# Kernel optimization log

Hardware: AMD Instinct MI355X
Metric: run time of the kernel (lower is better)

The kernel has to match this reference:

```python
import jax, jax.numpy as jnp
import numpy as np

IN_FEATS = 768   # xlm-roberta-base hidden size
HIDDEN = 128     # hardcoded in GCNEncoder
OUT_FEATS = 128
NUM_GRAPHS = 1024
NODES_PER_GRAPH = 256
N = NUM_GRAPHS * NODES_PER_GRAPH
N_CLASS = 2


def setup_inputs() -> dict:
    key = jax.random.key(0)
    ks = jax.random.split(key, 12)
    s = lambda fan_in: 1.0 / np.sqrt(fan_in)
    return {
        "x": jax.random.normal(ks[0], (N, IN_FEATS), dtype=jnp.float32),
        "prompt_node": jax.random.normal(ks[1], (IN_FEATS,), dtype=jnp.float32),
        "class_nodes": jax.random.normal(ks[2], (N_CLASS, IN_FEATS), dtype=jnp.float32),
        "W1": jax.random.uniform(ks[3], (IN_FEATS, HIDDEN), jnp.float32, -s(IN_FEATS), s(IN_FEATS)),
        "b1": jnp.zeros((HIDDEN,), jnp.float32),
        "W2": jax.random.uniform(ks[4], (HIDDEN, OUT_FEATS), jnp.float32, -s(HIDDEN), s(HIDDEN)),
        "b2": jnp.zeros((OUT_FEATS,), jnp.float32),
        "Wfc": jax.random.uniform(ks[5], (OUT_FEATS, N_CLASS), jnp.float32, -s(OUT_FEATS), s(OUT_FEATS)),
        "bfc": jnp.zeros((N_CLASS,), jnp.float32),
        "num_graphs": NUM_GRAPHS,
    }


def _gcn_conv(h_in, W, b, src, dst, num_nodes):
    # PyG GCNConv: add self loops, symmetric norm D^-1/2 (A+I) D^-1/2, then X W + b.
    deg = jax.ops.segment_sum(jnp.ones_like(src, dtype=h_in.dtype), dst,
                              num_segments=num_nodes) + 1.0  # +1 for self loop
    dinv = deg ** -0.5
    h = h_in @ W                                    # [num_nodes, out]
    norm = dinv[src] * dinv[dst]                    # [E]
    agg = jax.ops.segment_sum(h[src] * norm[:, None], dst, num_segments=num_nodes)
    agg = agg + (dinv * dinv)[:, None] * h          # self-loop contribution
    return agg + b


def reference(x, prompt_node, class_nodes, W1, b1, W2, b2, Wfc, bfc, num_graphs):
    G = int(num_graphs)
    N_orig = x.shape[0]
    n_per = N_orig // G
    n_cls = class_nodes.shape[0]
    total = N_orig + G + G * n_cls

    # construct_prompted_graph: append prompt nodes then class nodes (tiled per graph)
    full_x = jnp.concatenate([
        x,
        jnp.broadcast_to(prompt_node, (G, prompt_node.shape[0])),
        jnp.tile(class_nodes, (G, 1)),
    ], axis=0)

    # star edges: node -> prompt, prompt -> class; then to_undirected (both dirs)
    src1 = jnp.arange(N_orig)
    dst1 = N_orig + jnp.repeat(jnp.arange(G), n_per)
    src2 = jnp.repeat(N_orig + jnp.arange(G), n_cls)
    dst2 = N_orig + G + jnp.arange(G * n_cls)
    src = jnp.concatenate([src1, src2, dst1, dst2])
    dst = jnp.concatenate([dst1, dst2, src1, src2])

    h = _gcn_conv(full_x, W1, b1, src, dst, total)
    h = jax.nn.relu(h)  # dropout omitted (eval mode)
    h = _gcn_conv(h, W2, b2, src, dst, total)

    class_idx = N_orig + G + jnp.arange(G * n_cls)
    class_emb = h[class_idx]                         # [G*n_cls, OUT_FEATS]
    logits = class_emb @ Wfc + bfc                   # [G*n_cls, 2]
    return jax.nn.log_softmax(logits, axis=-1)
```

## Files before the change

### kernel.cpp

```cpp
#include <hip/hip_runtime.h>
#include <math.h>

namespace {
constexpr int IN_FEATS = 768;
constexpr int HIDDEN   = 128;
constexpr int G        = 1024;
constexpr int NPG      = 256;
constexpr int C4       = IN_FEATS / 4;
constexpr int NT       = 384;
constexpr int GPB      = 2;
constexpr int NB       = G / GPB;
typedef float f32x4 __attribute__((ext_vector_type(4)));
}

__global__ __launch_bounds__(NT, 3) void fused_kernel(
    const float* __restrict__ x, const float* __restrict__ prompt,
    const float* __restrict__ cls,
    const float* __restrict__ W1, const float* __restrict__ b1,
    const float* __restrict__ W2, const float* __restrict__ b2,
    const float* __restrict__ Wfc, const float* __restrict__ bfc,
    float* __restrict__ out)
{
    __shared__ __align__(16) float S[GPB][IN_FEATS];
    __shared__ f32x4  partA[2][C4];
    __shared__ float  pb[3][5][HIDDEN];
    __shared__ __align__(16) float rbuf[4][HIDDEN];
    __shared__ float  red[2][2];

    const int g0  = blockIdx.x * GPB;
    const int tid = threadIdx.x;
    const float ainv = 1.0f / sqrtf(518.0f);

    const int p  = tid / C4;
    const int c4 = tid % C4;
    const f32x4* xb = reinterpret_cast<const f32x4*>(x);
    for (int gg = 0; gg < GPB; ++gg) {
        const f32x4* xp = xb + ((size_t)(g0 + gg) * NPG + p) * C4 + c4;
        f32x4 a0 = (f32x4)0.0f;
        f32x4 a1 = a0, a2 = a0, a3 = a0;
        for (int i = 0; i < NPG / 2; i += 4) {
            const f32x4 v0 = __builtin_nontemporal_load(xp + (size_t)(2 * (i + 0)) * C4);
            const f32x4 v1 = __builtin_nontemporal_load(xp + (size_t)(2 * (i + 1)) * C4);
            const f32x4 v2 = __builtin_nontemporal_load(xp + (size_t)(2 * (i + 2)) * C4);
            const f32x4 v3 = __builtin_nontemporal_load(xp + (size_t)(2 * (i + 3)) * C4);
            a0 += v0; a1 += v1; a2 += v2; a3 += v3;
        }
        partA[p][c4] = (a0 + a1) + (a2 + a3);
        __syncthreads();
        if (tid < C4) {
            const f32x4 q0 = partA[0][tid], q1 = partA[1][tid];
            *reinterpret_cast<f32x4*>(&S[gg][tid * 4]) = q0 + q1;
        }
        __syncthreads();
    }

    {
        const int seg = tid >> 7;
        const int j   = tid & (HIDDEN - 1);
        const int cb  = seg * 256;
        const float* w1p = W1 + (size_t)cb * HIDDEN + j;
        float t0 = 0.f, t1 = 0.f, hp = 0.f, h0 = 0.f, h1 = 0.f;
        for (int cc = 0; cc < 256; cc += 4) {
            const int c = cb + cc;
            const f32x4 s0 = *reinterpret_cast<const f32x4*>(&S[0][c]);
            const f32x4 s1 = *reinterpret_cast<const f32x4*>(&S[1][c]);
            const f32x4 pv = *reinterpret_cast<const f32x4*>(prompt + c);
            const f32x4 k0 = *reinterpret_cast<const f32x4*>(cls + c);
            const f32x4 k1 = *reinterpret_cast<const f32x4*>(cls + IN_FEATS + c);
            const float w0 = w1p[(size_t)(cc + 0) * HIDDEN];
            const float w1 = w1p[(size_t)(cc + 1) * HIDDEN];
            const float w2 = w1p[(size_t)(cc + 2) * HIDDEN];
            const float w3 = w1p[(size_t)(cc + 3) * HIDDEN];
            t0 = fmaf(s0.x, w0, t0); t1 = fmaf(s1.x, w0, t1);
            hp = fmaf(pv.x, w0, hp); h0 = fmaf(k0.x, w0, h0); h1 = fmaf(k1.x, w0, h1);
            t0 = fmaf(s0.y, w1, t0); t1 = fmaf(s1.y, w1, t1);
            hp = fmaf(pv.y, w1, hp); h0 = fmaf(k0.y, w1, h0); h1 = fmaf(k1.y, w1, h1);
            t0 = fmaf(s0.z, w2, t0); t1 = fmaf(s1.z, w2, t1);
            hp = fmaf(pv.z, w2, hp); h0 = fmaf(k0.z, w2, h0); h1 = fmaf(k1.z, w2, h1);
            t0 = fmaf(s0.w, w3, t0); t1 = fmaf(s1.w, w3, t1);
            hp = fmaf(pv.w, w3, hp); h0 = fmaf(k0.w, w3, h0); h1 = fmaf(k1.w, w3, h1);
        }
        pb[seg][0][j] = t0; pb[seg][1][j] = t1;
        pb[seg][2][j] = hp; pb[seg][3][j] = h0; pb[seg][4][j] = h1;
    }
    __syncthreads();
    if (tid < HIDDEN) {
        const float t0 = pb[0][0][tid] + pb[1][0][tid] + pb[2][0][tid];
        const float t1 = pb[0][1][tid] + pb[1][1][tid] + pb[2][1][tid];
        const float hp = pb[0][2][tid] + pb[1][2][tid] + pb[2][2][tid];
        const float h0 = pb[0][3][tid] + pb[1][3][tid] + pb[2][3][tid];
        const float h1 = pb[0][4][tid] + pb[1][4][tid] + pb[2][4][tid];
        const float b  = b1[tid];
        const float C1 = ainv * (h0 + h1) + hp * (1.0f / 259.0f) + b;
        rbuf[0][tid] = fmaxf(fmaf(ainv, t0, C1), 0.f);
        rbuf[1][tid] = fmaxf(fmaf(ainv, t1, C1), 0.f);
        rbuf[2][tid] = fmaxf(fmaf(ainv, hp, fmaf(0.5f, h0, b)), 0.f);
        rbuf[3][tid] = fmaxf(fmaf(ainv, hp, fmaf(0.5f, h1, b)), 0.f);
    }
    __syncthreads();

    float u0 = 0.f, u1 = 0.f, uc0 = 0.f, uc1 = 0.f;
    if (tid < HIDDEN) {
        const float* w2p = W2 + tid;
        for (int c = 0; c < HIDDEN; c += 4) {
            const f32x4 r0 = *reinterpret_cast<const f32x4*>(&rbuf[0][c]);
            const f32x4 r1 = *reinterpret_cast<const f32x4*>(&rbuf[1][c]);
            const f32x4 q0 = *reinterpret_cast<const f32x4*>(&rbuf[2][c]);
            const f32x4 q1 = *reinterpret_cast<const f32x4*>(&rbuf[3][c]);
            const float wa = w2p[(size_t)(c + 0) * HIDDEN];
            const float wb = w2p[(size_t)(c + 1) * HIDDEN];
            const float wc = w2p[(size_t)(c + 2) * HIDDEN];
            const float wd = w2p[(size_t)(c + 3) * HIDDEN];
            u0  = fmaf(r0.x, wa, u0);  u1  = fmaf(r1.x, wa, u1);
            uc0 = fmaf(q0.x, wa, uc0); uc1 = fmaf(q1.x, wa, uc1);
            u0  = fmaf(r0.y, wb, u0);  u1  = fmaf(r1.y, wb, u1);
            uc0 = fmaf(q0.y, wb, uc0); uc1 = fmaf(q1.y, wb, uc1);
            u0  = fmaf(r0.z, wc, u0);  u1  = fmaf(r1.z, wc, u1);
            uc0 = fmaf(q0.z, wc, uc0); uc1 = fmaf(q1.z, wc, uc1);
            u0  = fmaf(r0.w, wd, u0);  u1  = fmaf(r1.w, wd, u1);
            uc0 = fmaf(q0.w, wd, uc0); uc1 = fmaf(q1.w, wd, uc1);
        }
    }

    const float bfc0 = bfc[0], bfc1 = bfc[1];
    for (int gg = 0; gg < GPB; ++gg) {
        for (int k = 0; k < 2; ++k) {
            float p0 = 0.f, p1 = 0.f;
            if (tid < HIDDEN) {
                const float ug = (gg == 0) ? u0 : u1;
                const float uk = (k == 0) ? uc0 : uc1;
                const float v  = fmaf(ainv, ug, fmaf(0.5f, uk, b2[tid]));
                p0 = v * Wfc[tid * 2 + 0];
                p1 = v * Wfc[tid * 2 + 1];
                #pragma unroll
                for (int off = 32; off > 0; off >>= 1) {
                    p0 += __shfl_down(p0, off);
                    p1 += __shfl_down(p1, off);
                }
                if ((tid & 63) == 0) { red[tid >> 6][0] = p0; red[tid >> 6][1] = p1; }
            }
            __syncthreads();
            if (tid == 0) {
                const float l0 = red[0][0] + red[1][0] + bfc0;
                const float l1 = red[0][1] + red[1][1] + bfc1;
                const float m   = fmaxf(l0, l1);
                const float lse = m + logf(expf(l0 - m) + expf(l1 - m));
                float* o = out + ((size_t)(g0 + gg) * 2 + k) * 2;
                o[0] = l0 - lse;
                o[1] = l1 - lse;
            }
            __syncthreads();
        }
    }
}

extern "C" void kernel_launch(void* const* d_in, const int* in_sizes, int n_in,
                              void* d_out, int out_size, void* d_ws, size_t ws_size,
                              hipStream_t stream) {
    const float* x      = (const float*)d_in[0];
    const float* prompt = (const float*)d_in[1];
    const float* cls    = (const float*)d_in[2];
    const float* W1     = (const float*)d_in[3];
    const float* b1     = (const float*)d_in[4];
    const float* W2     = (const float*)d_in[5];
    const float* b2     = (const float*)d_in[6];
    const float* Wfc    = (const float*)d_in[7];
    const float* bfc    = (const float*)d_in[8];
    float* out = (float*)d_out;

    fused_kernel<<<NB, NT, 0, stream>>>(x, prompt, cls, W1, b1, W2, b2,
                                        Wfc, bfc, out);
}
```

Baseline: 145.5 us.

## Add dedicated compute warps to overlap W1 GEMV with streaming of next graph

The block grows from 384 to 512 threads: 384 threads stream and reduce the node features while 128 extra threads compute the layer-1 projections. The projection for graph 0, prompt and class nodes runs while the streamers read graph 1, and only graph 1's projection remains after the streaming. This hides part of the W1 matrix-vector work behind the memory-bound reduction. The cost is more threads per block and occupancy hint 4, a serial 768-length dot product per compute thread instead of a 3-way split, and a tail GEMV still exposed for the second graph.

```diff
diff --git a/kernel.cpp b/kernel.cpp
--- a/kernel.cpp
+++ b/kernel.cpp
@@ -7,37 +7,39 @@
 constexpr int G        = 1024;
 constexpr int NPG      = 256;
 constexpr int C4       = IN_FEATS / 4;
-constexpr int NT       = 384;
+constexpr int NSTREAM  = 384;
+constexpr int NT       = 512;
 constexpr int GPB      = 2;
 constexpr int NB       = G / GPB;
 typedef float f32x4 __attribute__((ext_vector_type(4)));
 }
 
-__global__ __launch_bounds__(NT, 3) void fused_kernel(
+__global__ __launch_bounds__(NT, 4) void fused_kernel(
     const float* __restrict__ x, const float* __restrict__ prompt,
     const float* __restrict__ cls,
-    const float* __restrict__ W1, const float* __restrict__ b1,
-    const float* __restrict__ W2, const float* __restrict__ b2,
+    const float* __restrict__ W1, const float* __restrict__ bias1,
+    const float* __restrict__ W2, const float* __restrict__ bias2,
     const float* __restrict__ Wfc, const float* __restrict__ bfc,
     float* __restrict__ out)
 {
     __shared__ __align__(16) float S[GPB][IN_FEATS];
     __shared__ f32x4  partA[2][C4];
-    __shared__ float  pb[3][5][HIDDEN];
+    __shared__ float  cb[5][HIDDEN];
     __shared__ __align__(16) float rbuf[4][HIDDEN];
     __shared__ float  red[2][2];
 
     const int g0  = blockIdx.x * GPB;
     const int tid = threadIdx.x;
     const float ainv = 1.0f / sqrtf(518.0f);
+    const bool streamer = tid < NSTREAM;
 
     const int p  = tid / C4;
     const int c4 = tid % C4;
     const f32x4* xb = reinterpret_cast<const f32x4*>(x);
-    for (int gg = 0; gg < GPB; ++gg) {
-        const f32x4* xp = xb + ((size_t)(g0 + gg) * NPG + p) * C4 + c4;
-        f32x4 a0 = (f32x4)0.0f;
-        f32x4 a1 = a0, a2 = a0, a3 = a0;
+
+    if (streamer) {
+        const f32x4* xp = xb + ((size_t)(g0 + 0) * NPG + p) * C4 + c4;
+        f32x4 a0 = (f32x4)0.0f, a1 = a0, a2 = a0, a3 = a0;
         for (int i = 0; i < NPG / 2; i += 4) {
             const f32x4 v0 = __builtin_nontemporal_load(xp + (size_t)(2 * (i + 0)) * C4);
             const f32x4 v1 = __builtin_nontemporal_load(xp + (size_t)(2 * (i + 1)) * C4);
@@ -46,51 +48,79 @@
             a0 += v0; a1 += v1; a2 += v2; a3 += v3;
         }
         partA[p][c4] = (a0 + a1) + (a2 + a3);
-        __syncthreads();
-        if (tid < C4) {
-            const f32x4 q0 = partA[0][tid], q1 = partA[1][tid];
-            *reinterpret_cast<f32x4*>(&S[gg][tid * 4]) = q0 + q1;
-        }
-        __syncthreads();
-    }
-
-    {
-        const int seg = tid >> 7;
-        const int j   = tid & (HIDDEN - 1);
-        const int cb  = seg * 256;
-        const float* w1p = W1 + (size_t)cb * HIDDEN + j;
-        float t0 = 0.f, t1 = 0.f, hp = 0.f, h0 = 0.f, h1 = 0.f;
-        for (int cc = 0; cc < 256; cc += 4) {
-            const int c = cb + cc;
+    }
+    __syncthreads();
+    if (tid < C4) {
+        const f32x4 q0 = partA[0][tid], q1 = partA[1][tid];
+        *reinterpret_cast<f32x4*>(&S[0][tid * 4]) = q0 + q1;
+    }
+    __syncthreads();
+
+    if (streamer) {
+        const f32x4* xp = xb + ((size_t)(g0 + 1) * NPG + p) * C4 + c4;
+        f32x4 a0 = (f32x4)0.0f, a1 = a0, a2 = a0, a3 = a0;
+        for (int i = 0; i < NPG / 2; i += 4) {
+            const f32x4 v0 = __builtin_nontemporal_load(xp + (size_t)(2 * (i + 0)) * C4);
+            const f32x4 v1 = __builtin_nontemporal_load(xp + (size_t)(2 * (i + 1)) * C4);
+            const f32x4 v2 = __builtin_nontemporal_load(xp + (size_t)(2 * (i + 2)) * C4);
+            const f32x4 v3 = __builtin_nontemporal_load(xp + (size_t)(2 * (i + 3)) * C4);
+            a0 += v0; a1 += v1; a2 += v2; a3 += v3;
+        }
+        partA[p][c4] = (a0 + a1) + (a2 + a3);
+    } else {
+        const int j = tid - NSTREAM;
+        const float* w1p = W1 + j;
+        float t0 = 0.f, hp = 0.f, h0 = 0.f, h1 = 0.f;
+        for (int c = 0; c < IN_FEATS; c += 4) {
             const f32x4 s0 = *reinterpret_cast<const f32x4*>(&S[0][c]);
-            const f32x4 s1 = *reinterpret_cast<const f32x4*>(&S[1][c]);
             const f32x4 pv = *reinterpret_cast<const f32x4*>(prompt + c);
             const f32x4 k0 = *reinterpret_cast<const f32x4*>(cls + c);
             const f32x4 k1 = *reinterpret_cast<const f32x4*>(cls + IN_FEATS + c);
-            const float w0 = w1p[(size_t)(cc + 0) * HIDDEN];
-            const float w1 = w1p[(size_t)(cc + 1) * HIDDEN];
-            const float w2 = w1p[(size_t)(cc + 2) * HIDDEN];
-            const float w3 = w1p[(size_t)(cc + 3) * HIDDEN];
-            t0 = fmaf(s0.x, w0, t0); t1 = fmaf(s1.x, w0, t1);
-            hp = fmaf(pv.x, w0, hp); h0 = fmaf(k0.x, w0, h0); h1 = fmaf(k1.x, w0, h1);
-            t0 = fmaf(s0.y, w1, t0); t1 = fmaf(s1.y, w1, t1);
-            hp = fmaf(pv.y, w1, hp); h0 = fmaf(k0.y, w1, h0); h1 = fmaf(k1.y, w1, h1);
-            t0 = fmaf(s0.z, w2, t0); t1 = fmaf(s1.z, w2, t1);
-            hp = fmaf(pv.z, w2, hp); h0 = fmaf(k0.z, w2, h0); h1 = fmaf(k1.z, w2, h1);
-            t0 = fmaf(s0.w, w3, t0); t1 = fmaf(s1.w, w3, t1);
-            hp = fmaf(pv.w, w3, hp); h0 = fmaf(k0.w, w3, h0); h1 = fmaf(k1.w, w3, h1);
-        }
-        pb[seg][0][j] = t0; pb[seg][1][j] = t1;
-        pb[seg][2][j] = hp; pb[seg][3][j] = h0; pb[seg][4][j] = h1;
-    }
-    __syncthreads();
+            const float w0 = w1p[(size_t)(c + 0) * HIDDEN];
+            const float w1 = w1p[(size_t)(c + 1) * HIDDEN];
+            const float w2 = w1p[(size_t)(c + 2) * HIDDEN];
+            const float w3 = w1p[(size_t)(c + 3) * HIDDEN];
+            t0 = fmaf(s0.x, w0, t0); hp = fmaf(pv.x, w0, hp);
+            h0 = fmaf(k0.x, w0, h0); h1 = fmaf(k1.x, w0, h1);
+            t0 = fmaf(s0.y, w1, t0); hp = fmaf(pv.y, w1, hp);
+            h0 = fmaf(k0.y, w1, h0); h1 = fmaf(k1.y, w1, h1);
+            t0 = fmaf(s0.z, w2, t0); hp = fmaf(pv.z, w2, hp);
+            h0 = fmaf(k0.z, w2, h0); h1 = fmaf(k1.z, w2, h1);
+            t0 = fmaf(s0.w, w3, t0); hp = fmaf(pv.w, w3, hp);
+            h0 = fmaf(k0.w, w3, h0); h1 = fmaf(k1.w, w3, h1);
+        }
+        cb[0][j] = t0; cb[2][j] = hp; cb[3][j] = h0; cb[4][j] = h1;
+    }
+    __syncthreads();
+    if (tid < C4) {
+        const f32x4 q0 = partA[0][tid], q1 = partA[1][tid];
+        *reinterpret_cast<f32x4*>(&S[1][tid * 4]) = q0 + q1;
+    }
+    __syncthreads();
+
+    if (!streamer) {
+        const int j = tid - NSTREAM;
+        const float* w1p = W1 + j;
+        float t1 = 0.f;
+        for (int c = 0; c < IN_FEATS; c += 4) {
+            const f32x4 s1 = *reinterpret_cast<const f32x4*>(&S[1][c]);
+            const float w0 = w1p[(size_t)(c + 0) * HIDDEN];
+            const float w1 = w1p[(size_t)(c + 1) * HIDDEN];
+            const float w2 = w1p[(size_t)(c + 2) * HIDDEN];
+            const float w3 = w1p[(size_t)(c + 3) * HIDDEN];
+            t1 = fmaf(s1.x, w0, t1);
+            t1 = fmaf(s1.y, w1, t1);
+            t1 = fmaf(s1.z, w2, t1);
+            t1 = fmaf(s1.w, w3, t1);
+        }
+        cb[1][j] = t1;
+    }
+    __syncthreads();
+
     if (tid < HIDDEN) {
-        const float t0 = pb[0][0][tid] + pb[1][0][tid] + pb[2][0][tid];
-        const float t1 = pb[0][1][tid] + pb[1][1][tid] + pb[2][1][tid];
-        const float hp = pb[0][2][tid] + pb[1][2][tid] + pb[2][2][tid];
-        const float h0 = pb[0][3][tid] + pb[1][3][tid] + pb[2][3][tid];
-        const float h1 = pb[0][4][tid] + pb[1][4][tid] + pb[2][4][tid];
-        const float b  = b1[tid];
+        const float t0 = cb[0][tid], t1 = cb[1][tid];
+        const float hp = cb[2][tid], h0 = cb[3][tid], h1 = cb[4][tid];
+        const float b  = bias1[tid];
         const float C1 = ainv * (h0 + h1) + hp * (1.0f / 259.0f) + b;
         rbuf[0][tid] = fmaxf(fmaf(ainv, t0, C1), 0.f);
         rbuf[1][tid] = fmaxf(fmaf(ainv, t1, C1), 0.f);
@@ -129,7 +159,7 @@
             if (tid < HIDDEN) {
                 const float ug = (gg == 0) ? u0 : u1;
                 const float uk = (k == 0) ? uc0 : uc1;
-                const float v  = fmaf(ainv, ug, fmaf(0.5f, uk, b2[tid]));
+                const float v  = fmaf(ainv, ug, fmaf(0.5f, uk, bias2[tid]));
                 p0 = v * Wfc[tid * 2 + 0];
                 p1 = v * Wfc[tid * 2 + 1];
                 #pragma unroll
```

Measured after the change: 145.8 us. No clear change (+0.2%).
